# Kernel optimization log

Hardware: AMD Instinct MI355X
Metric: run time of the kernel (lower is better)

Reference implementation:

```python
import jax, jax.numpy as jnp
import numpy as np

N_NODES = 50000
N_EDGES = 800000
IN_CH = 256
HID = 256
OUT_CH = 128


def setup_inputs() -> dict:
    key = jax.random.key(0)
    ks = jax.random.split(key, 12)
    x = jax.random.normal(ks[0], (N_NODES, IN_CH), dtype=jnp.float32)
    adj_rows = jnp.sort(jax.random.randint(ks[1], (N_EDGES,), 0, N_NODES, dtype=jnp.int32))
    adj_cols = jax.random.randint(ks[2], (N_EDGES,), 0, N_NODES, dtype=jnp.int32)
    # normalized adjacency weights (~1/degree scale)
    adj_vals = jax.random.uniform(ks[3], (N_EDGES,), dtype=jnp.float32) / 16.0
    def xavier(k, fan_in, fan_out):
        lim = float(np.sqrt(6.0 / (fan_in + fan_out)))
        return jax.random.uniform(k, (fan_in, fan_out), dtype=jnp.float32, minval=-lim, maxval=lim)
    Wa0 = xavier(ks[4], IN_CH, HID)
    Wa1 = xavier(ks[5], HID, HID)
    Wl0 = xavier(ks[6], IN_CH + HID, HID)
    Wl1 = xavier(ks[7], 2 * HID, OUT_CH)
    return {
        'x': x, 'adj_rows': adj_rows, 'adj_cols': adj_cols, 'adj_vals': adj_vals,
        'Wa0': Wa0, 'ba0': jnp.zeros((HID,), jnp.float32),
        'Wa1': Wa1, 'ba1': jnp.zeros((HID,), jnp.float32),
        'Wl0': Wl0, 'bl0': jnp.zeros((HID,), jnp.float32),
        'Wl1': Wl1, 'bl1': jnp.zeros((OUT_CH,), jnp.float32),
    }


def reference(x, adj_rows, adj_cols, adj_vals, Wa0, ba0, Wa1, ba1, Wl0, bl0, Wl1, bl1):
    n = x.shape[0]

    def spmm(h):
        # sparse adj @ h : gather neighbor rows, scale by edge weight, segment-sum into dst
        return jax.ops.segment_sum(adj_vals[:, None] * h[adj_cols], adj_rows, num_segments=n)

    # layer 0
    agg = jax.nn.relu(spmm(x) @ Wa0 + ba0)
    h = jax.nn.relu(jnp.concatenate((x, agg), axis=1) @ Wl0 + bl0)
    # layer 1 (last: no activation after linear)
    agg = jax.nn.relu(spmm(h) @ Wa1 + ba1)
    h = jnp.concatenate((h, agg), axis=1) @ Wl1 + bl1
    # F.normalize: row-wise L2 with eps=1e-12
    norm = jnp.maximum(jnp.linalg.norm(h, axis=1, keepdims=True), 1e-12)
    return h / norm
```

## Files before the change

kernel.cpp:

```cpp
#include <hip/hip_runtime.h>

typedef unsigned short u16;
typedef __attribute__((ext_vector_type(8))) __bf16 bf16x8;
typedef __attribute__((ext_vector_type(4))) float f32x4;
typedef __attribute__((ext_vector_type(8))) u16 u16x8;
typedef __attribute__((ext_vector_type(4))) u16 u16x4;

__device__ __forceinline__ float bf2f(u16 u) {
  return __builtin_bit_cast(float, ((unsigned)u) << 16);
}
__device__ __forceinline__ u16 f2bf(float f) {
  unsigned x = __builtin_bit_cast(unsigned, f);
  x += 0x7fffu + ((x >> 16) & 1u);
  return (u16)(x >> 16);
}
__device__ __forceinline__ f32x4 cvt4(u16x4 v) {
  return (f32x4){bf2f(v.x), bf2f(v.y), bf2f(v.z), bf2f(v.w)};
}
__device__ __forceinline__ void gload_lds16(const void* g, void* l) {
  __builtin_amdgcn_global_load_lds(
      (const __attribute__((address_space(1))) void*)g,
      (__attribute__((address_space(3))) void*)l, 16, 0, 0);
}

__global__ void prepw4_kernel(const float* __restrict__ W0, u16* __restrict__ T0,
                              const float* __restrict__ W1, u16* __restrict__ T1,
                              const float* __restrict__ W2, u16* __restrict__ T2,
                              const float* __restrict__ W3, u16* __restrict__ T3) {
  int i = blockIdx.x * 256 + threadIdx.x;
  const float* W; u16* T; int K, N;
  if (i < 65536)        { W = W0; T = T0; K = 256; N = 256; }
  else if (i < 131072)  { W = W1; T = T1; K = 256; N = 256; i -= 65536; }
  else if (i < 262144)  { W = W2; T = T2; K = 512; N = 256; i -= 131072; }
  else if (i < 327680)  { W = W3; T = T3; K = 512; N = 128; i -= 262144; }
  else return;
  int k = i / N, n = i - k * N;
  T[(size_t)n * K + k] = f2bf(W[i]);
}

__global__ void cvtx_kernel(const float* __restrict__ in, u16* __restrict__ out,
                            int total4) {
  int i = blockIdx.x * 256 + threadIdx.x;
  if (i >= total4) return;
  const float4 v = ((const float4*)in)[i];
  u16x4 o = { f2bf(v.x), f2bf(v.y), f2bf(v.z), f2bf(v.w) };
  ((u16x4*)out)[i] = o;
}

__global__ void rowptr_kernel(const int* __restrict__ rows, int nE,
                              int* __restrict__ rp, int nN) {
  int i = blockIdx.x * 256 + threadIdx.x;
  if (i > nN) return;
  int lo = 0, hi = nE;
  while (lo < hi) { int mid = (lo + hi) >> 1; if (rows[mid] < i) lo = mid + 1; else hi = mid; }
  rp[i] = lo;
}

__global__ __launch_bounds__(256) void spmm_kernel(
    const u16* __restrict__ X, const int* __restrict__ rp,
    const int* __restrict__ cols, const float* __restrict__ vals,
    u16* __restrict__ out, int nN) {
  int lane = threadIdx.x & 63;
  int node = blockIdx.x * 4 + (threadIdx.x >> 6);
  if (node >= nN) return;
  int e0 = rp[node], e1 = rp[node + 1];
  f32x4 s[8];
  #pragma unroll
  for (int i = 0; i < 8; ++i) s[i] = (f32x4){0.f, 0.f, 0.f, 0.f};
  const u16* xp = X + (size_t)lane * 4;
  const int elast = e1 - 1;
  for (int base = e0; base < e1; base += 16) {
    int c[16]; float v[16];
    #pragma unroll
    for (int i = 0; i < 16; ++i) {
      int idx = base + i;
      bool ok = idx < e1;
      int j = ok ? idx : elast;
      c[i] = cols[j];
      v[i] = ok ? vals[j] : 0.f;
    }
    u16x4 xv[16];
    #pragma unroll
    for (int i = 0; i < 16; ++i) xv[i] = *(const u16x4*)(xp + (size_t)c[i] * 256);
    #pragma unroll
    for (int i = 0; i < 16; ++i) s[i & 7] += v[i] * cvt4(xv[i]);
  }
  f32x4 t = ((s[0] + s[1]) + (s[2] + s[3])) + ((s[4] + s[5]) + (s[6] + s[7]));
  u16x4 o = { f2bf(t.x), f2bf(t.y), f2bf(t.z), f2bf(t.w) };
  *(u16x4*)(out + (size_t)node * 256 + lane * 4) = o;
}

template<int KTOT, bool SPLIT, bool RELU, bool OUTF32, bool NORM>
__global__ __launch_bounds__(256) void gemm_kernel(
    const u16* __restrict__ A0, const u16* __restrict__ A1,
    const u16* __restrict__ Wt, const float* __restrict__ bias,
    void* __restrict__ outp, int M, int N) {
  __shared__ u16 As[128 * 64];
  __shared__ u16 Bs[128 * 64];
  __shared__ float red[128][2];

  const int lane = threadIdx.x & 63;
  const int wid = threadIdx.x >> 6;
  const int wr = wid >> 1, wc = wid & 1;
  const int row0b = blockIdx.y * 128;
  const int col0b = blockIdx.x * 128;
  const int lr = lane & 15;
  const int kg = lane >> 4;

  const int u = (wid * 4) * 64 + lane;
  f32x4 acc[4][4];
  #pragma unroll
  for (int ni = 0; ni < 4; ++ni) {
    float bv = bias[col0b + wc * 64 + ni * 16 + lr];
    #pragma unroll
    for (int mi = 0; mi < 4; ++mi) acc[mi][ni] = (f32x4){bv, bv, bv, bv};
  }

  constexpr int KSTEPS = KTOT / 64;
  for (int kt = 0; kt < KSTEPS; ++kt) {
    const u16* Asrc = (!SPLIT || kt < 4) ? A0 : A1;
    const int kkl = (!SPLIT || kt < 4) ? kt * 64 : (kt - 4) * 64;

    if (kt) __syncthreads();
    #pragma unroll
    for (int i = 0; i < 4; ++i) {
      const int c = wid * 4 + i;
      const int uu = u + i * 64;
      const int row = uu >> 3;
      const int ksd = uu & 7;
      const int kss = ksd ^ (row & 7);
      int grow = row0b + row;
      if (grow >= M) grow = M - 1;
      gload_lds16(Asrc + (size_t)grow * 256 + kkl + kss * 8, &As[c * 512]);
      gload_lds16(Wt + (size_t)(col0b + row) * KTOT + kt * 64 + kss * 8, &Bs[c * 512]);
    }
    __syncthreads();

    #pragma unroll
    for (int ks = 0; ks < 2; ++ks) {
      const int q = ks * 4 + kg;
      bf16x8 a[4], b[4];
      #pragma unroll
      for (int mi = 0; mi < 4; ++mi) {
        const int r = wr * 64 + mi * 16 + lr;
        a[mi] = __builtin_bit_cast(bf16x8,
            *(const u16x8*)&As[r * 64 + (q ^ (r & 7)) * 8]);
      }
      #pragma unroll
      for (int ni = 0; ni < 4; ++ni) {
        const int cb = wc * 64 + ni * 16 + lr;
        b[ni] = __builtin_bit_cast(bf16x8,
            *(const u16x8*)&Bs[cb * 64 + (q ^ (cb & 7)) * 8]);
      }
      #pragma unroll
      for (int mi = 0; mi < 4; ++mi)
        #pragma unroll
        for (int ni = 0; ni < 4; ++ni)
          acc[mi][ni] = __builtin_amdgcn_mfma_f32_16x16x32_bf16(a[mi], b[ni], acc[mi][ni], 0, 0, 0);
    }
  }

  float invn[4][4];
  if (NORM) {
    #pragma unroll
    for (int mi = 0; mi < 4; ++mi) {
      #pragma unroll
      for (int j = 0; j < 4; ++j) {
        float p = 0.f;
        #pragma unroll
        for (int ni = 0; ni < 4; ++ni) { float v = acc[mi][ni][j]; p += v * v; }
        #pragma unroll
        for (int m = 1; m < 16; m <<= 1) p += __shfl_xor(p, m, 64);
        int rl = wr * 64 + mi * 16 + kg * 4 + j;
        if (lr == 0) red[rl][wc] = p;
        invn[mi][j] = 0.f;
      }
    }
    __syncthreads();
    #pragma unroll
    for (int mi = 0; mi < 4; ++mi) {
      #pragma unroll
      for (int j = 0; j < 4; ++j) {
        int rl = wr * 64 + mi * 16 + kg * 4 + j;
        float ss = red[rl][0] + red[rl][1];
        float nrm = sqrtf(ss);
        nrm = nrm > 1e-12f ? nrm : 1e-12f;
        invn[mi][j] = 1.f / nrm;
      }
    }
  }

  #pragma unroll
  for (int mi = 0; mi < 4; ++mi) {
    #pragma unroll
    for (int j = 0; j < 4; ++j) {
      int r = row0b + wr * 64 + mi * 16 + kg * 4 + j;
      if (r >= M) continue;
      #pragma unroll
      for (int ni = 0; ni < 4; ++ni) {
        float v = acc[mi][ni][j];
        if (RELU) v = v > 0.f ? v : 0.f;
        if (NORM) v *= invn[mi][j];
        int c = col0b + wc * 64 + ni * 16 + lr;
        if (OUTF32) ((float*)outp)[(size_t)r * N + c] = v;
        else        ((u16*)outp)[(size_t)r * N + c] = f2bf(v);
      }
    }
  }
}

extern "C" void kernel_launch(void* const* d_in, const int* in_sizes, int n_in,
                              void* d_out, int out_size, void* d_ws, size_t ws_size,
                              hipStream_t stream) {
  const float* x        = (const float*)d_in[0];
  const int*   adj_rows = (const int*)d_in[1];
  const int*   adj_cols = (const int*)d_in[2];
  const float* adj_vals = (const float*)d_in[3];
  const float* Wa0 = (const float*)d_in[4];
  const float* ba0 = (const float*)d_in[5];
  const float* Wa1 = (const float*)d_in[6];
  const float* ba1 = (const float*)d_in[7];
  const float* Wl0 = (const float*)d_in[8];
  const float* bl0 = (const float*)d_in[9];
  const float* Wl1 = (const float*)d_in[10];
  const float* bl1 = (const float*)d_in[11];

  const int nN = in_sizes[0] / 256;
  const int nE = in_sizes[1];

  char* ws = (char*)d_ws;
  size_t off = 0;
  auto alloc = [&](size_t bytes) -> void* {
    void* p = ws + off;
    off += (bytes + 255) & ~(size_t)255;
    return p;
  };
  u16* x_bf  = (u16*)alloc((size_t)nN * 256 * 2);
  u16* aggA  = (u16*)alloc((size_t)nN * 256 * 2);
  u16* aggB  = (u16*)alloc((size_t)nN * 256 * 2);
  u16* h_bf  = (u16*)alloc((size_t)nN * 256 * 2);
  int* rp    = (int*)alloc((size_t)(nN + 1) * 4);
  u16* wt_a0 = (u16*)alloc(256 * 256 * 2);
  u16* wt_a1 = (u16*)alloc(256 * 256 * 2);
  u16* wt_l0 = (u16*)alloc(512 * 256 * 2);
  u16* wt_l1 = (u16*)alloc(512 * 128 * 2);
  if (off > ws_size) return;

  dim3 blk(256);
  prepw4_kernel<<<dim3(1280), blk, 0, stream>>>(Wa0, wt_a0, Wa1, wt_a1, Wl0, wt_l0, Wl1, wt_l1);
  cvtx_kernel<<<dim3((nN * 64 + 255) / 256), blk, 0, stream>>>(x, x_bf, nN * 64);
  rowptr_kernel<<<dim3((nN + 1 + 255) / 256), blk, 0, stream>>>(adj_rows, nE, rp, nN);

  const int MB = (nN + 127) / 128;
  dim3 gN256(2, MB);
  dim3 gN128(1, MB);
  dim3 gNode((nN + 3) / 4);

  spmm_kernel<<<gNode, blk, 0, stream>>>(x_bf, rp, adj_cols, adj_vals, aggA, nN);
  gemm_kernel<256, false, true, false, false><<<gN256, blk, 0, stream>>>(aggA, nullptr, wt_a0, ba0, aggB, nN, 256);
  gemm_kernel<512, true, true, false, false><<<gN256, blk, 0, stream>>>(x_bf, aggB, wt_l0, bl0, h_bf, nN, 256);
  spmm_kernel<<<gNode, blk, 0, stream>>>(h_bf, rp, adj_cols, adj_vals, aggA, nN);
  gemm_kernel<256, false, true, false, false><<<gN256, blk, 0, stream>>>(aggA, nullptr, wt_a1, ba1, aggB, nN, 256);
  gemm_kernel<512, true, false, true, true><<<gN128, blk, 0, stream>>>(h_bf, aggB, wt_l1, bl1, (float*)d_out, nN, 128);
}
```

Measured before the change: 242.6 us.

## Double-buffer GEMM LDS tiles and simplify SpMM gather loop with smaller blocks

The GEMM kernel now keeps two LDS buffers for A and B and issues the next k-tile's global-to-LDS loads before computing on the current tile, so load latency can overlap with MFMA work. The SpMM kernel drops its 16-wide padded gather batch for a 4-wide unrolled loop plus a remainder loop, and moves to 128-thread blocks with 2 nodes each. Double buffering doubles LDS use per block, which may reduce occupancy. Relying on one barrier per iteration with async LDS loads may also be a correctness risk if outstanding loads are not waited on. The narrower SpMM unroll exposes less memory-level parallelism per wave.

```diff
diff --git a/kernel.cpp b/kernel.cpp
--- a/kernel.cpp
+++ b/kernel.cpp
@@ -56,37 +56,37 @@
   rp[i] = lo;
 }
 
-__global__ __launch_bounds__(256) void spmm_kernel(
+__global__ __launch_bounds__(128) void spmm_kernel(
     const u16* __restrict__ X, const int* __restrict__ rp,
     const int* __restrict__ cols, const float* __restrict__ vals,
     u16* __restrict__ out, int nN) {
   int lane = threadIdx.x & 63;
-  int node = blockIdx.x * 4 + (threadIdx.x >> 6);
+  int node = blockIdx.x * 2 + (threadIdx.x >> 6);
   if (node >= nN) return;
   int e0 = rp[node], e1 = rp[node + 1];
-  f32x4 s[8];
-  #pragma unroll
-  for (int i = 0; i < 8; ++i) s[i] = (f32x4){0.f, 0.f, 0.f, 0.f};
+  f32x4 s0 = {0.f, 0.f, 0.f, 0.f}, s1 = s0, s2 = s0, s3 = s0;
   const u16* xp = X + (size_t)lane * 4;
-  const int elast = e1 - 1;
-  for (int base = e0; base < e1; base += 16) {
-    int c[16]; float v[16];
-    #pragma unroll
-    for (int i = 0; i < 16; ++i) {
-      int idx = base + i;
-      bool ok = idx < e1;
-      int j = ok ? idx : elast;
-      c[i] = cols[j];
-      v[i] = ok ? vals[j] : 0.f;
-    }
-    u16x4 xv[16];
-    #pragma unroll
-    for (int i = 0; i < 16; ++i) xv[i] = *(const u16x4*)(xp + (size_t)c[i] * 256);
-    #pragma unroll
-    for (int i = 0; i < 16; ++i) s[i & 7] += v[i] * cvt4(xv[i]);
-  }
-  f32x4 t = ((s[0] + s[1]) + (s[2] + s[3])) + ((s[4] + s[5]) + (s[6] + s[7]));
-  u16x4 o = { f2bf(t.x), f2bf(t.y), f2bf(t.z), f2bf(t.w) };
+  int e = e0;
+  for (; e + 4 <= e1; e += 4) {
+    int c0 = cols[e], c1 = cols[e + 1], c2 = cols[e + 2], c3 = cols[e + 3];
+    float v0 = vals[e], v1 = vals[e + 1], v2 = vals[e + 2], v3 = vals[e + 3];
+    u16x4 x0 = *(const u16x4*)(xp + (size_t)c0 * 256);
+    u16x4 x1 = *(const u16x4*)(xp + (size_t)c1 * 256);
+    u16x4 x2 = *(const u16x4*)(xp + (size_t)c2 * 256);
+    u16x4 x3 = *(const u16x4*)(xp + (size_t)c3 * 256);
+    s0 += v0 * cvt4(x0);
+    s1 += v1 * cvt4(x1);
+    s2 += v2 * cvt4(x2);
+    s3 += v3 * cvt4(x3);
+  }
+  for (; e < e1; ++e) {
+    int c = cols[e];
+    float v = vals[e];
+    u16x4 xv = *(const u16x4*)(xp + (size_t)c * 256);
+    s0 += v * cvt4(xv);
+  }
+  f32x4 s = (s0 + s1) + (s2 + s3);
+  u16x4 o = { f2bf(s.x), f2bf(s.y), f2bf(s.z), f2bf(s.w) };
   *(u16x4*)(out + (size_t)node * 256 + lane * 4) = o;
 }
 
@@ -95,8 +95,8 @@
     const u16* __restrict__ A0, const u16* __restrict__ A1,
     const u16* __restrict__ Wt, const float* __restrict__ bias,
     void* __restrict__ outp, int M, int N) {
-  __shared__ u16 As[128 * 64];
-  __shared__ u16 Bs[128 * 64];
+  __shared__ u16 As[2][128 * 64];
+  __shared__ u16 Bs[2][128 * 64];
   __shared__ float red[128][2];
 
   const int lane = threadIdx.x & 63;
@@ -108,20 +108,10 @@
   const int kg = lane >> 4;
 
   const int u = (wid * 4) * 64 + lane;
-  f32x4 acc[4][4];
-  #pragma unroll
-  for (int ni = 0; ni < 4; ++ni) {
-    float bv = bias[col0b + wc * 64 + ni * 16 + lr];
-    #pragma unroll
-    for (int mi = 0; mi < 4; ++mi) acc[mi][ni] = (f32x4){bv, bv, bv, bv};
-  }
-
-  constexpr int KSTEPS = KTOT / 64;
-  for (int kt = 0; kt < KSTEPS; ++kt) {
+
+  auto stage = [&](int buf, int kt) {
     const u16* Asrc = (!SPLIT || kt < 4) ? A0 : A1;
     const int kkl = (!SPLIT || kt < 4) ? kt * 64 : (kt - 4) * 64;
-
-    if (kt) __syncthreads();
     #pragma unroll
     for (int i = 0; i < 4; ++i) {
       const int c = wid * 4 + i;
@@ -131,10 +121,26 @@
       const int kss = ksd ^ (row & 7);
       int grow = row0b + row;
       if (grow >= M) grow = M - 1;
-      gload_lds16(Asrc + (size_t)grow * 256 + kkl + kss * 8, &As[c * 512]);
-      gload_lds16(Wt + (size_t)(col0b + row) * KTOT + kt * 64 + kss * 8, &Bs[c * 512]);
-    }
-    __syncthreads();
+      gload_lds16(Asrc + (size_t)grow * 256 + kkl + kss * 8, &As[buf][c * 512]);
+      gload_lds16(Wt + (size_t)(col0b + row) * KTOT + kt * 64 + kss * 8, &Bs[buf][c * 512]);
+    }
+  };
+
+  f32x4 acc[4][4];
+  #pragma unroll
+  for (int ni = 0; ni < 4; ++ni) {
+    float bv = bias[col0b + wc * 64 + ni * 16 + lr];
+    #pragma unroll
+    for (int mi = 0; mi < 4; ++mi) acc[mi][ni] = (f32x4){bv, bv, bv, bv};
+  }
+
+  constexpr int KSTEPS = KTOT / 64;
+  stage(0, 0);
+  __syncthreads();
+
+  for (int kt = 0; kt < KSTEPS; ++kt) {
+    const int cur = kt & 1;
+    if (kt + 1 < KSTEPS) stage(cur ^ 1, kt + 1);
 
     #pragma unroll
     for (int ks = 0; ks < 2; ++ks) {
@@ -144,13 +150,13 @@
       for (int mi = 0; mi < 4; ++mi) {
         const int r = wr * 64 + mi * 16 + lr;
         a[mi] = __builtin_bit_cast(bf16x8,
-            *(const u16x8*)&As[r * 64 + (q ^ (r & 7)) * 8]);
+            *(const u16x8*)&As[cur][r * 64 + (q ^ (r & 7)) * 8]);
       }
       #pragma unroll
       for (int ni = 0; ni < 4; ++ni) {
         const int cb = wc * 64 + ni * 16 + lr;
         b[ni] = __builtin_bit_cast(bf16x8,
-            *(const u16x8*)&Bs[cb * 64 + (q ^ (cb & 7)) * 8]);
+            *(const u16x8*)&Bs[cur][cb * 64 + (q ^ (cb & 7)) * 8]);
       }
       #pragma unroll
       for (int mi = 0; mi < 4; ++mi)
@@ -158,6 +164,7 @@
         for (int ni = 0; ni < 4; ++ni)
           acc[mi][ni] = __builtin_amdgcn_mfma_f32_16x16x32_bf16(a[mi], b[ni], acc[mi][ni], 0, 0, 0);
     }
+    __syncthreads();
   }
 
   float invn[4][4];
@@ -254,12 +261,13 @@
   const int MB = (nN + 127) / 128;
   dim3 gN256(2, MB);
   dim3 gN128(1, MB);
-  dim3 gNode((nN + 3) / 4);
-
-  spmm_kernel<<<gNode, blk, 0, stream>>>(x_bf, rp, adj_cols, adj_vals, aggA, nN);
+  dim3 gNode((nN + 1) / 2);
+  dim3 sblk(128);
+
+  spmm_kernel<<<gNode, sblk, 0, stream>>>(x_bf, rp, adj_cols, adj_vals, aggA, nN);
   gemm_kernel<256, false, true, false, false><<<gN256, blk, 0, stream>>>(aggA, nullptr, wt_a0, ba0, aggB, nN, 256);
   gemm_kernel<512, true, true, false, false><<<gN256, blk, 0, stream>>>(x_bf, aggB, wt_l0, bl0, h_bf, nN, 256);
-  spmm_kernel<<<gNode, blk, 0, stream>>>(h_bf, rp, adj_cols, adj_vals, aggA, nN);
+  spmm_kernel<<<gNode, sblk, 0, stream>>>(h_bf, rp, adj_cols, adj_vals, aggA, nN);
   gemm_kernel<256, false, true, false, false><<<gN256, blk, 0, stream>>>(aggA, nullptr, wt_a1, ba1, aggB, nN, 256);
   gemm_kernel<512, true, false, true, true><<<gN128, blk, 0, stream>>>(h_bf, aggB, wt_l1, bl1, (float*)d_out, nN, 128);
 }
```

After: 227.3 us. 6.3% less time.
